# Performance work log

Hardware: AMD Instinct MI355X
Metric: run time of the kernel (lower is better)

The kernel has to match this reference:

```python
import math
import jax, jax.numpy as jnp
import numpy as np

B, S, E, H = 2, 2048, 1024, 16
DK = E // H

def setup_inputs() -> dict:
    key = jax.random.key(0)
    ks = jax.random.split(key, 12)
    sc = 1.0 / math.sqrt(E)
    return {
        "x": jax.random.normal(ks[0], (B, S, E), jnp.float32),
        "kv": jax.random.normal(ks[1], (B, S, E), jnp.float32),
        "mask": jax.random.randint(ks[2], (B, S), 0, 2, jnp.int32),
        "attn_bias": jax.random.normal(ks[3], (B, S, S), jnp.float32),
        "WQ_w": jax.random.normal(ks[4], (E, E), jnp.float32) * sc,
        "WQ_b": jnp.zeros((E,), jnp.float32),
        "WK_w": jax.random.normal(ks[5], (E, E), jnp.float32) * sc,
        "WK_b": jnp.zeros((E,), jnp.float32),
        "WV_w": jax.random.normal(ks[6], (E, E), jnp.float32) * sc,
        "WV_b": jnp.zeros((E,), jnp.float32),
        "WO_w": jax.random.normal(ks[7], (E, E), jnp.float32) * sc,
        "WO_b": jnp.zeros((E,), jnp.float32),
    }

def reference(x, kv, mask, attn_bias, WQ_w, WQ_b, WK_w, WK_b, WV_w, WV_b, WO_w, WO_b):
    b, sq, _ = x.shape
    sk = kv.shape[1]
    # projections, split heads: [B,S,E] -> [B,H,S,DK]
    Q = (x @ WQ_w.T + WQ_b).reshape(b, sq, H, DK).transpose(0, 2, 1, 3)
    K = (kv @ WK_w.T + WK_b).reshape(b, sk, H, DK).transpose(0, 2, 1, 3)
    V = (kv @ WV_w.T + WV_b).reshape(b, sk, H, DK).transpose(0, 2, 1, 3)
    # scores [B,H,Sq,Sk]
    T = jnp.einsum('bhqd,bhkd->bhqk', Q, K) / math.sqrt(DK)
    T = T + attn_bias[:, None, :, :]  # 3D bias broadcast over heads
    m2 = jnp.einsum('bi,bj->bij', mask.astype(T.dtype), mask.astype(T.dtype))
    T = jnp.where(m2[:, None, :, :] == 0, jnp.asarray(-1e9, T.dtype), T)
    A = jax.nn.softmax(T, axis=-1)
    out = jnp.einsum('bhqk,bhkd->bhqd', A, V)  # [B,H,Sq,DK]
    out = out.transpose(0, 2, 1, 3).reshape(b, sq, E)
    return out @ WO_w.T + WO_b
```

## Files before the change

### kernel.cpp

```cpp
#include <hip/hip_runtime.h>

#define DEV static __device__ __forceinline__

typedef __attribute__((ext_vector_type(8))) __bf16 bf16x8;
typedef __attribute__((ext_vector_type(4))) float f32x4;

constexpr int CB = 2;
constexpr int CS = 2048;
constexpr int CE = 1024;
constexpr int CH = 16;
constexpr int CD = 64;
constexpr float LOG2E = 1.44269504f;

DEV unsigned short f2bf(float x) {
  unsigned int u = __float_as_uint(x);
  u += 0x7fffu + ((u >> 16) & 1u);
  return (unsigned short)(u >> 16);
}

DEV f32x4 mfma32(bf16x8 a, bf16x8 b, f32x4 c) {
  return __builtin_amdgcn_mfma_f32_16x16x32_bf16(a, b, c, 0, 0, 0);
}

DEV unsigned int cvtpk(float lo, float hi) {
  unsigned int r;
  asm("v_cvt_pk_bf16_f32 %0, %1, %2" : "=v"(r) : "v"(lo), "v"(hi));
  return r;
}

DEV float exp2r(float x) {
#if __has_builtin(__builtin_amdgcn_exp2f)
  return __builtin_amdgcn_exp2f(x);
#else
  float r; asm("v_exp_f32 %0, %1" : "=v"(r) : "v"(x)); return r;
#endif
}

DEV f32x4 unpk(unsigned int a, unsigned int b) {
  f32x4 r;
  r[0] = __uint_as_float(a << 16);
  r[1] = __uint_as_float(a & 0xffff0000u);
  r[2] = __uint_as_float(b << 16);
  r[3] = __uint_as_float(b & 0xffff0000u);
  return r;
}

DEV void stage16(const void* g, void* l) {
  __builtin_amdgcn_global_load_lds(
      (const __attribute__((address_space(1))) unsigned int*)g,
      (__attribute__((address_space(3))) unsigned int*)l, 16, 0, 0);
}

DEV void wcvt_body(long i, const float* __restrict__ w0, const float* __restrict__ w1,
                   const float* __restrict__ w2, const float* __restrict__ w3,
                   unsigned short* __restrict__ out) {
  const long WE = (long)CE * CE;
  const int wi = (int)(i >> 20);
  const float* src = wi == 0 ? w0 : wi == 1 ? w1 : wi == 2 ? w2 : w3;
  const long off = i & (WE - 1);
  float4 a = *reinterpret_cast<const float4*>(src + off);
  float4 b = *reinterpret_cast<const float4*>(src + off + 4);
  uint4 v;
  v.x = cvtpk(a.x, a.y); v.y = cvtpk(a.z, a.w);
  v.z = cvtpk(b.x, b.y); v.w = cvtpk(b.z, b.w);
  *reinterpret_cast<uint4*>(out + i) = v;
}

DEV void mbias_body(long idx, const float* __restrict__ bias, const int* __restrict__ mask,
                    unsigned short* __restrict__ mb16) {
  const int b = (int)(idx >> 22);
  const int q = (int)((idx >> 11) & (CS - 1));
  const int k0 = (int)(idx & (CS - 1));
  const bool mq = mask[b * CS + q] != 0;
  const int4 mk0 = *reinterpret_cast<const int4*>(mask + b * CS + k0);
  const int4 mk1 = *reinterpret_cast<const int4*>(mask + b * CS + k0 + 4);
  const float4 b0 = *reinterpret_cast<const float4*>(bias + idx);
  const float4 b1 = *reinterpret_cast<const float4*>(bias + idx + 4);
  const float NEG = -1e9f * LOG2E;
  float v[8];
  if (mq) {
    v[0] = (mk0.x != 0) ? b0.x * LOG2E : NEG;
    v[1] = (mk0.y != 0) ? b0.y * LOG2E : NEG;
    v[2] = (mk0.z != 0) ? b0.z * LOG2E : NEG;
    v[3] = (mk0.w != 0) ? b0.w * LOG2E : NEG;
    v[4] = (mk1.x != 0) ? b1.x * LOG2E : NEG;
    v[5] = (mk1.y != 0) ? b1.y * LOG2E : NEG;
    v[6] = (mk1.z != 0) ? b1.z * LOG2E : NEG;
    v[7] = (mk1.w != 0) ? b1.w * LOG2E : NEG;
  } else {
#pragma unroll
    for (int j = 0; j < 8; j++) v[j] = 0.f;
  }
  uint4 o;
  o.x = cvtpk(v[0], v[1]); o.y = cvtpk(v[2], v[3]);
  o.z = cvtpk(v[4], v[5]); o.w = cvtpk(v[6], v[7]);
  *reinterpret_cast<uint4*>(mb16 + idx) = o;
}

__global__ __launch_bounds__(256) void prep_all(const float* __restrict__ w0,
                                                const float* __restrict__ w1,
                                                const float* __restrict__ w2,
                                                const float* __restrict__ w3,
                                                unsigned short* __restrict__ wout,
                                                const float* __restrict__ bias,
                                                const int* __restrict__ mask,
                                                unsigned short* __restrict__ mb16) {
  const long WCB = (4L * CE * CE) / 2048;
  if (blockIdx.x < WCB) {
    wcvt_body(((long)blockIdx.x * 256 + threadIdx.x) * 8, w0, w1, w2, w3, wout);
  } else {
    mbias_body(((long)(blockIdx.x - WCB) * 256 + threadIdx.x) * 8, bias, mask, mb16);
  }
}

__global__ __launch_bounds__(512) void gemm_qkv(const float* __restrict__ xf,
                                                const float* __restrict__ kvf,
                                                const unsigned short* __restrict__ Wall,
                                                const float* __restrict__ bq,
                                                const float* __restrict__ bk,
                                                const float* __restrict__ bv,
                                                unsigned short* __restrict__ Qb) {
  __shared__ __align__(16) unsigned char ldsA[32768];
  __shared__ __align__(16) unsigned char ldsB[32768];
  const long NE = (long)CB * CS * CE;
  const long WE = (long)CE * CE;
  const int which = blockIdx.y >> 2;
  const int n0 = (blockIdx.y & 3) * 256;
  const int m0 = blockIdx.x * 256;
  const float* Ax = which == 0 ? xf : kvf;
  const unsigned char* Bb = (const unsigned char*)(Wall + (long)which * WE);
  const float* bias = which == 0 ? bq : which == 1 ? bk : bv;

  const int tid = threadIdx.x;
  const int lane = tid & 63, w = tid >> 6;
  const int wr = w >> 2, wc = w & 3;
  const int g = lane >> 4, rr = lane & 15;

  const int srow = tid >> 2;
  const int ecol = ((tid & 3) * 8) ^ (((tid >> 5) & 1) * 16);
  const float* afp0 = Ax + (long)(m0 + srow) * CE + ecol;
  const float* afp1 = Ax + (long)(m0 + 128 + srow) * CE + ecol;
  const float* afb0 = afp0;
  const float* afb1 = afp1;
  const int scsw = ((tid & 3) * 16) ^ (((tid >> 5) & 1) << 5);
  const unsigned char* bpR0 = Bb + ((long)(n0 + srow) * CE) * 2 + scsw;
  const unsigned char* bpR1 = Bb + ((long)(n0 + 128 + srow) * CE) * 2 + scsw;

  const int cswz = (g * 16) ^ (((rr >> 3) & 1) << 5);
  const unsigned char* rbA = ldsA + wr * 8192 + rr * 64 + cswz;
  const unsigned char* rbB = ldsB + wc * 4096 + rr * 64 + cswz;

  f32x4 acc[8][4] = {};
  float4 afr0, afr1, afr2, afr3;

  auto loadA = [&](bool junk) {
    const float* p0 = junk ? afb0 : afp0;
    const float* p1 = junk ? afb1 : afp1;
    afr0 = *reinterpret_cast<const float4*>(p0);
    afr1 = *reinterpret_cast<const float4*>(p0 + 4);
    afr2 = *reinterpret_cast<const float4*>(p1);
    afr3 = *reinterpret_cast<const float4*>(p1 + 4);
    if (!junk) { afp0 += 32; afp1 += 32; }
  };
  auto writeA = [&](int buf) {
    uint4 w0v, w1v;
    w0v.x = cvtpk(afr0.x, afr0.y); w0v.y = cvtpk(afr0.z, afr0.w);
    w0v.z = cvtpk(afr1.x, afr1.y); w0v.w = cvtpk(afr1.z, afr1.w);
    w1v.x = cvtpk(afr2.x, afr2.y); w1v.y = cvtpk(afr2.z, afr2.w);
    w1v.z = cvtpk(afr3.x, afr3.y); w1v.w = cvtpk(afr3.z, afr3.w);
    *reinterpret_cast<uint4*>(ldsA + buf * 16384 + tid * 16) = w0v;
    *reinterpret_cast<uint4*>(ldsA + buf * 16384 + 8192 + tid * 16) = w1v;
  };
  auto stB = [&](int buf) {
    stage16(bpR0, ldsB + buf * 16384 + w * 1024);
    stage16(bpR1, ldsB + buf * 16384 + 8192 + w * 1024);
    bpR0 += 64; bpR1 += 64;
  };

  loadA(false);
  stB(0);
  asm volatile("s_waitcnt vmcnt(2)" ::: "memory");
  writeA(0);
  loadA(false);
  stB(1);
  asm volatile("s_waitcnt vmcnt(6)" ::: "memory");
  asm volatile("s_waitcnt lgkmcnt(0)" ::: "memory");
  __builtin_amdgcn_s_barrier();

  auto group = [&](int buf, bool junk) {
    bf16x8 ar[4], br[4];
#pragma unroll
    for (int ii = 0; ii < 4; ii++)
      ar[ii] = *reinterpret_cast<const bf16x8*>(rbA + buf * 16384 + ii * 1024);
#pragma unroll
    for (int j = 0; j < 4; j++)
      br[j] = *reinterpret_cast<const bf16x8*>(rbB + buf * 16384 + j * 1024);
    asm volatile("s_waitcnt vmcnt(2)" ::: "memory");
    writeA(buf ^ 1);
    loadA(junk);
    asm volatile("s_waitcnt lgkmcnt(0)" ::: "memory");
    __builtin_amdgcn_sched_barrier(0);
    __builtin_amdgcn_s_setprio(1);
#pragma unroll
    for (int ii = 0; ii < 4; ii++)
#pragma unroll
      for (int j = 0; j < 4; j++)
        acc[ii][j] = mfma32(ar[ii], br[j], acc[ii][j]);
    __builtin_amdgcn_s_setprio(0);
    __builtin_amdgcn_s_barrier();
#pragma unroll
    for (int ii = 0; ii < 4; ii++)
      ar[ii] = *reinterpret_cast<const bf16x8*>(rbA + buf * 16384 + 4096 + ii * 1024);
    stB(buf);
    asm volatile("s_waitcnt lgkmcnt(0)" ::: "memory");
    __builtin_amdgcn_sched_barrier(0);
    __builtin_amdgcn_s_setprio(1);
#pragma unroll
    for (int ii = 0; ii < 4; ii++)
#pragma unroll
      for (int j = 0; j < 4; j++)
        acc[4 + ii][j] = mfma32(ar[ii], br[j], acc[4 + ii][j]);
    __builtin_amdgcn_s_setprio(0);
    asm volatile("s_waitcnt vmcnt(6)" ::: "memory");
    __builtin_amdgcn_s_barrier();
  };

#pragma unroll 1
  for (int it = 0; it < 16; ++it) {
    group(0, it == 15);
    group(1, it == 15);
  }
  asm volatile("s_waitcnt vmcnt(0)" ::: "memory");

  const float scale = which == 0 ? 0.125f * LOG2E : 1.0f;
#pragma unroll
  for (int i = 0; i < 8; i++) {
#pragma unroll
    for (int j = 0; j < 4; j++) {
      const int colg = n0 + wc * 64 + j * 16 + rr;
      const float bvv = bias[colg];
      if (which == 2) {
        const int rowbase = m0 + wr * 128 + i * 16 + g * 4;
        const int bb = rowbase >> 11, s = rowbase & 2047;
        const int hh = colg >> 6, d = colg & 63;
        uint2 val;
        val.x = (unsigned int)f2bf(acc[i][j][0] + bvv) | ((unsigned int)f2bf(acc[i][j][1] + bvv) << 16);
        val.y = (unsigned int)f2bf(acc[i][j][2] + bvv) | ((unsigned int)f2bf(acc[i][j][3] + bvv) << 16);
        *reinterpret_cast<uint2*>(Qb + 2 * NE + ((long)((bb * CH + hh) * CD + d)) * CS + s) = val;
      } else {
        unsigned short* outp = Qb + (long)which * NE;
#pragma unroll
        for (int r = 0; r < 4; r++) {
          const int row = m0 + wr * 128 + i * 16 + g * 4 + r;
          outp[(long)row * CE + colg] = f2bf((acc[i][j][r] + bvv) * scale);
        }
      }
    }
  }
}

__global__ __launch_bounds__(256) void gemm_wo(const unsigned short* __restrict__ A,
                                               const unsigned short* __restrict__ W,
                                               const float* __restrict__ bias,
                                               float* __restrict__ out) {
  __shared__ __align__(16) unsigned short As[128 * 64];
  __shared__ __align__(16) unsigned short Bs[64 * 64];
  const int tid = threadIdx.x;
  const int lane = tid & 63, wave = tid >> 6;
  const int wm = (wave >> 1) * 64, wn = (wave & 1) * 32;
  const int g = lane >> 4, rr = lane & 15;
  const int m0 = blockIdx.x * 128, n0 = blockIdx.y * 64;
  const int K = CE;
  f32x4 acc[4][2] = {};

  for (int k0 = 0; k0 < K; k0 += 64) {
#pragma unroll
    for (int t = 0; t < 4; t++) {
      const int u = t * 256 + tid;
      const int row = u >> 3, ce = (u & 7) * 8;
      stage16(A + (long)(m0 + row) * K + k0 + ce, (char*)As + (t * 256 + (tid & 192)) * 16);
    }
#pragma unroll
    for (int t = 0; t < 2; t++) {
      const int u = t * 256 + tid;
      const int row = u >> 3, ce = (u & 7) * 8;
      stage16(W + (long)(n0 + row) * K + k0 + ce, (char*)Bs + (t * 256 + (tid & 192)) * 16);
    }
    __syncthreads();
#pragma unroll
    for (int kk = 0; kk < 2; kk++) {
      bf16x8 af[4], bfr[2];
#pragma unroll
      for (int i = 0; i < 4; i++)
        af[i] = *reinterpret_cast<const bf16x8*>(&As[(wm + i * 16 + rr) * 64 + kk * 32 + g * 8]);
#pragma unroll
      for (int j = 0; j < 2; j++)
        bfr[j] = *reinterpret_cast<const bf16x8*>(&Bs[(wn + j * 16 + rr) * 64 + kk * 32 + g * 8]);
#pragma unroll
      for (int i = 0; i < 4; i++)
#pragma unroll
        for (int j = 0; j < 2; j++)
          acc[i][j] = mfma32(af[i], bfr[j], acc[i][j]);
    }
    __syncthreads();
  }

#pragma unroll
  for (int i = 0; i < 4; i++)
#pragma unroll
    for (int j = 0; j < 2; j++) {
      const int colg = n0 + wn + j * 16 + rr;
      const float bvv = bias[colg];
#pragma unroll
      for (int r = 0; r < 4; r++) {
        const int row = m0 + wm + i * 16 + g * 4 + r;
        out[(long)row * CE + colg] = acc[i][j][r] + bvv;
      }
    }
}

__global__ __launch_bounds__(256, 2) void attn_kernel(const unsigned short* __restrict__ Qb,
                                                      const unsigned short* __restrict__ Kb,
                                                      const unsigned short* __restrict__ Vtw,
                                                      const unsigned short* __restrict__ mb16,
                                                      const int* __restrict__ mask,
                                                      unsigned short* __restrict__ AO) {
  __shared__ __align__(16) unsigned char lds[65536];
  const int h = blockIdx.x, qt = blockIdx.y, b = blockIdx.z;
  const int tid = threadIdx.x;
  const int lane = tid & 63, w = tid >> 6;
  const int g = lane >> 4, c = lane & 15;
  const int qbase = qt * 128 + w * 32;

  bf16x8 qf[2][2];
#pragma unroll
  for (int qb = 0; qb < 2; qb++) {
    const unsigned short* Qrow = Qb + ((long)b * CS + qbase + qb * 16 + c) * CE + h * CD;
    qf[qb][0] = *reinterpret_cast<const bf16x8*>(Qrow + g * 8);
    qf[qb][1] = *reinterpret_cast<const bf16x8*>(Qrow + 32 + g * 8);
    if (mask[b * CS + qbase + qb * 16 + c] == 0) {
      qf[qb][0] = bf16x8{}; qf[qb][1] = bf16x8{};
    }
  }

  const unsigned char *kg[4], *vg[4];
  {
    const unsigned char* Ksrc = (const unsigned char*)(Kb + (long)b * CS * CE + h * CD);
    const unsigned char* Vsrc = (const unsigned char*)(Vtw + (long)(b * CH + h) * CD * CS);
    const int rr8 = lane >> 3;
    const int csw = ((lane & 7) << 4) ^ (rr8 << 4);
#pragma unroll
    for (int t = 0; t < 4; t++) {
      const int krow = t * 32 + w * 8 + rr8;
      const int key = (krow & 96) + ((krow >> 2) & 3) * 8 + ((krow >> 4) & 1) * 4 + (krow & 3);
      kg[t] = Ksrc + (long)key * (CE * 2) + csw;
      const int vrow = (t & 1) * 32 + w * 8 + rr8;
      vg[t] = Vsrc + (long)vrow * (CS * 2) + (t >> 1) * 128 + csw;
    }
  }
  const int sw = (c & 7) << 4;
  const unsigned char* rb0 = lds + c * 128 + ((g * 16) ^ sw);
  const unsigned char* rb1 = lds + c * 128 + ((64 + g * 16) ^ sw);

  const unsigned short* mbp0 = mb16 + ((long)b * CS + qbase + c) * CS + g * 8;
  const unsigned short* mbp1 = mb16 + ((long)b * CS + qbase + 16 + c) * CS + g * 8;

  f32x4 o[2][4] = {};
  f32x4 lsum4[2] = {};
  uint4 mbr[2][4];

  auto stage = [&](int bo) {
    unsigned char* kbuf = lds + bo;
    unsigned char* vbuf = lds + bo + 16384;
#pragma unroll
    for (int t = 0; t < 4; t++) {
      stage16(kg[t], kbuf + t * 4096 + w * 1024);
      stage16(vg[t], vbuf + (t >> 1) * 8192 + (t & 1) * 4096 + w * 1024);
      kg[t] += 128 * CE * 2;
      vg[t] += 128 * 2;
    }
  };
  auto load_mb = [&](bool adv) {
#pragma unroll
    for (int kb = 0; kb < 4; kb++) {
      mbr[0][kb] = *reinterpret_cast<const uint4*>(mbp0 + kb * 32);
      mbr[1][kb] = *reinterpret_cast<const uint4*>(mbp1 + kb * 32);
    }
    if (adv) { mbp0 += 128; mbp1 += 128; }
  };

  auto compute = [&](int bo, bool adv) {
    f32x4 sf[2][8];
    __builtin_amdgcn_s_setprio(1);
#pragma unroll
    for (int cb = 0; cb < 8; cb++) {
      const bf16x8 kf0 = *reinterpret_cast<const bf16x8*>(rb0 + bo + cb * 2048);
      const bf16x8 kf1 = *reinterpret_cast<const bf16x8*>(rb1 + bo + cb * 2048);
#pragma unroll
      for (int qb = 0; qb < 2; qb++) {
        const uint4 m = mbr[qb][cb >> 1];
        const f32x4 ci = (cb & 1) ? unpk(m.z, m.w) : unpk(m.x, m.y);
        f32x4 t = mfma32(kf0, qf[qb][0], ci);
        sf[qb][cb] = mfma32(kf1, qf[qb][1], t);
      }
    }
    __builtin_amdgcn_s_setprio(0);
    load_mb(adv);
    uint4 pw[2][4];
#pragma unroll
    for (int qb = 0; qb < 2; qb++)
#pragma unroll
      for (int kb = 0; kb < 4; kb++)
#pragma unroll
        for (int half = 0; half < 2; half++) {
          const int cb = 2 * kb + half;
          f32x4 pv;
          pv[0] = exp2r(sf[qb][cb][0]);
          pv[1] = exp2r(sf[qb][cb][1]);
          pv[2] = exp2r(sf[qb][cb][2]);
          pv[3] = exp2r(sf[qb][cb][3]);
          lsum4[qb] = lsum4[qb] + pv;
          if (half == 0) { pw[qb][kb].x = cvtpk(pv[0], pv[1]); pw[qb][kb].y = cvtpk(pv[2], pv[3]); }
          else           { pw[qb][kb].z = cvtpk(pv[0], pv[1]); pw[qb][kb].w = cvtpk(pv[2], pv[3]); }
        }
    __builtin_amdgcn_s_setprio(1);
#pragma unroll
    for (int nb = 0; nb < 4; nb++) {
#pragma unroll
      for (int kb = 0; kb < 4; kb++) {
        const unsigned char* rbx = (kb & 1) ? rb1 : rb0;
        const bf16x8 vf = *reinterpret_cast<const bf16x8*>(
            rbx + bo + 16384 + (kb >> 1) * 8192 + nb * 2048);
#pragma unroll
        for (int qb = 0; qb < 2; qb++)
          o[qb][nb] = mfma32(vf, __builtin_bit_cast(bf16x8, pw[qb][kb]), o[qb][nb]);
      }
    }
    __builtin_amdgcn_s_setprio(0);
  };

  stage(0);
  load_mb(true);
  stage(32768);

#pragma unroll 1
  for (int it = 0; it < 8; ++it) {
    asm volatile("s_waitcnt vmcnt(16)" ::: "memory");
    __builtin_amdgcn_s_barrier();
    __builtin_amdgcn_sched_barrier(0);
    compute(0, it < 7);
    __builtin_amdgcn_sched_barrier(0);
    __builtin_amdgcn_s_barrier();
    stage(0);
    asm volatile("s_waitcnt vmcnt(16)" ::: "memory");
    __builtin_amdgcn_s_barrier();
    __builtin_amdgcn_sched_barrier(0);
    compute(32768, it < 7);
    __builtin_amdgcn_sched_barrier(0);
    __builtin_amdgcn_s_barrier();
    stage(32768);
  }

#pragma unroll
  for (int qb = 0; qb < 2; qb++) {
    float lsum = (lsum4[qb][0] + lsum4[qb][1]) + (lsum4[qb][2] + lsum4[qb][3]);
    lsum += __shfl_xor(lsum, 16, 64);
    lsum += __shfl_xor(lsum, 32, 64);
    const float linv = 1.0f / lsum;
    unsigned short* Orow = AO + ((long)b * CS + qbase + qb * 16 + c) * CE + h * CD;
#pragma unroll
    for (int nb = 0; nb < 4; nb++) {
      uint2 val;
      val.x = (unsigned int)f2bf(o[qb][nb][0] * linv) | ((unsigned int)f2bf(o[qb][nb][1] * linv) << 16);
      val.y = (unsigned int)f2bf(o[qb][nb][2] * linv) | ((unsigned int)f2bf(o[qb][nb][3] * linv) << 16);
      *reinterpret_cast<uint2*>(Orow + nb * 16 + g * 4) = val;
    }
  }
  asm volatile("s_waitcnt vmcnt(0)" ::: "memory");
}

extern "C" void kernel_launch(void* const* d_in, const int* in_sizes, int n_in,
                              void* d_out, int out_size, void* d_ws, size_t ws_size,
                              hipStream_t stream) {
  (void)in_sizes; (void)n_in; (void)out_size; (void)ws_size;
  const float* x    = (const float*)d_in[0];
  const float* kv   = (const float*)d_in[1];
  const int*   mask = (const int*)d_in[2];
  const float* ab   = (const float*)d_in[3];
  const float* WQw  = (const float*)d_in[4];
  const float* WQb  = (const float*)d_in[5];
  const float* WKw  = (const float*)d_in[6];
  const float* WKb  = (const float*)d_in[7];
  const float* WVw  = (const float*)d_in[8];
  const float* WVb  = (const float*)d_in[9];
  const float* WOw  = (const float*)d_in[10];
  const float* WOb  = (const float*)d_in[11];
  float* out = (float*)d_out;

  const long NE = (long)CB * CS * CE;
  const long WE = (long)CE * CE;
  unsigned short* ws  = (unsigned short*)d_ws;
  unsigned short* wqb = ws;
  unsigned short* wob = wqb + 3 * WE;
  unsigned short* Qb  = wob + WE;
  unsigned short* AO  = Qb + 3 * NE;
  unsigned short* mb16 = AO + NE;

  const long WCE = 4 * WE;
  const long MBE = (long)CB * CS * CS;

  prep_all<<<(int)((WCE + MBE) / 2048), 256, 0, stream>>>(WQw, WKw, WVw, WOw, wqb,
                                                          ab, mask, mb16);

  gemm_qkv<<<dim3(16, 12), 512, 0, stream>>>(x, kv, wqb, WQb, WKb, WVb, Qb);

  attn_kernel<<<dim3(CH, CS / 128, CB), 256, 0, stream>>>(
      Qb, Qb + NE, Qb + 2 * NE, mb16, mask, AO);

  gemm_wo<<<dim3(32, 16), 256, 0, stream>>>(AO, wob, WOb, out);
}
```

Baseline: 132.0 us.

## Fuse mask and bias into attention kernel, dropping the precomputed bf16 bias buffer

Removes the prep pass that built a pre-scaled, pre-masked bf16 bias matrix. The attention kernel now reads the fp32 attention bias and the key mask directly and applies the scale, mask and query-mask select before exp2, instead of seeding the MFMA accumulator with the bias. This saves one full write and read of a B×S×S buffer plus its prep launch. In exchange, every head block now reads fp32 bias, twice the bytes of bf16, and does extra ALU work per score. The prefetch and wait schedule for the bias loads is also simplified, so load latency may be exposed inside compute.

```diff
diff --git a/kernel.cpp b/kernel.cpp
--- a/kernel.cpp
+++ b/kernel.cpp
@@ -36,25 +36,19 @@
 #endif
 }
 
-DEV f32x4 unpk(unsigned int a, unsigned int b) {
-  f32x4 r;
-  r[0] = __uint_as_float(a << 16);
-  r[1] = __uint_as_float(a & 0xffff0000u);
-  r[2] = __uint_as_float(b << 16);
-  r[3] = __uint_as_float(b & 0xffff0000u);
-  return r;
-}
-
 DEV void stage16(const void* g, void* l) {
   __builtin_amdgcn_global_load_lds(
       (const __attribute__((address_space(1))) unsigned int*)g,
       (__attribute__((address_space(3))) unsigned int*)l, 16, 0, 0);
 }
 
-DEV void wcvt_body(long i, const float* __restrict__ w0, const float* __restrict__ w1,
-                   const float* __restrict__ w2, const float* __restrict__ w3,
-                   unsigned short* __restrict__ out) {
+__global__ __launch_bounds__(256) void wcvt_all(const float* __restrict__ w0,
+                                                const float* __restrict__ w1,
+                                                const float* __restrict__ w2,
+                                                const float* __restrict__ w3,
+                                                unsigned short* __restrict__ out) {
   const long WE = (long)CE * CE;
+  const long i = ((long)blockIdx.x * 256 + threadIdx.x) * 8;
   const int wi = (int)(i >> 20);
   const float* src = wi == 0 ? w0 : wi == 1 ? w1 : wi == 2 ? w2 : w3;
   const long off = i & (WE - 1);
@@ -64,53 +58,6 @@
   v.x = cvtpk(a.x, a.y); v.y = cvtpk(a.z, a.w);
   v.z = cvtpk(b.x, b.y); v.w = cvtpk(b.z, b.w);
   *reinterpret_cast<uint4*>(out + i) = v;
-}
-
-DEV void mbias_body(long idx, const float* __restrict__ bias, const int* __restrict__ mask,
-                    unsigned short* __restrict__ mb16) {
-  const int b = (int)(idx >> 22);
-  const int q = (int)((idx >> 11) & (CS - 1));
-  const int k0 = (int)(idx & (CS - 1));
-  const bool mq = mask[b * CS + q] != 0;
-  const int4 mk0 = *reinterpret_cast<const int4*>(mask + b * CS + k0);
-  const int4 mk1 = *reinterpret_cast<const int4*>(mask + b * CS + k0 + 4);
-  const float4 b0 = *reinterpret_cast<const float4*>(bias + idx);
-  const float4 b1 = *reinterpret_cast<const float4*>(bias + idx + 4);
-  const float NEG = -1e9f * LOG2E;
-  float v[8];
-  if (mq) {
-    v[0] = (mk0.x != 0) ? b0.x * LOG2E : NEG;
-    v[1] = (mk0.y != 0) ? b0.y * LOG2E : NEG;
-    v[2] = (mk0.z != 0) ? b0.z * LOG2E : NEG;
-    v[3] = (mk0.w != 0) ? b0.w * LOG2E : NEG;
-    v[4] = (mk1.x != 0) ? b1.x * LOG2E : NEG;
-    v[5] = (mk1.y != 0) ? b1.y * LOG2E : NEG;
-    v[6] = (mk1.z != 0) ? b1.z * LOG2E : NEG;
-    v[7] = (mk1.w != 0) ? b1.w * LOG2E : NEG;
-  } else {
-#pragma unroll
-    for (int j = 0; j < 8; j++) v[j] = 0.f;
-  }
-  uint4 o;
-  o.x = cvtpk(v[0], v[1]); o.y = cvtpk(v[2], v[3]);
-  o.z = cvtpk(v[4], v[5]); o.w = cvtpk(v[6], v[7]);
-  *reinterpret_cast<uint4*>(mb16 + idx) = o;
-}
-
-__global__ __launch_bounds__(256) void prep_all(const float* __restrict__ w0,
-                                                const float* __restrict__ w1,
-                                                const float* __restrict__ w2,
-                                                const float* __restrict__ w3,
-                                                unsigned short* __restrict__ wout,
-                                                const float* __restrict__ bias,
-                                                const int* __restrict__ mask,
-                                                unsigned short* __restrict__ mb16) {
-  const long WCB = (4L * CE * CE) / 2048;
-  if (blockIdx.x < WCB) {
-    wcvt_body(((long)blockIdx.x * 256 + threadIdx.x) * 8, w0, w1, w2, w3, wout);
-  } else {
-    mbias_body(((long)(blockIdx.x - WCB) * 256 + threadIdx.x) * 8, bias, mask, mb16);
-  }
 }
 
 __global__ __launch_bounds__(512) void gemm_qkv(const float* __restrict__ xf,
@@ -322,7 +269,7 @@
 __global__ __launch_bounds__(256, 2) void attn_kernel(const unsigned short* __restrict__ Qb,
                                                       const unsigned short* __restrict__ Kb,
                                                       const unsigned short* __restrict__ Vtw,
-                                                      const unsigned short* __restrict__ mb16,
+                                                      const float* __restrict__ bias,
                                                       const int* __restrict__ mask,
                                                       unsigned short* __restrict__ AO) {
   __shared__ __align__(16) unsigned char lds[65536];
@@ -333,14 +280,14 @@
   const int qbase = qt * 128 + w * 32;
 
   bf16x8 qf[2][2];
+  bool mq[2];
 #pragma unroll
   for (int qb = 0; qb < 2; qb++) {
     const unsigned short* Qrow = Qb + ((long)b * CS + qbase + qb * 16 + c) * CE + h * CD;
     qf[qb][0] = *reinterpret_cast<const bf16x8*>(Qrow + g * 8);
     qf[qb][1] = *reinterpret_cast<const bf16x8*>(Qrow + 32 + g * 8);
-    if (mask[b * CS + qbase + qb * 16 + c] == 0) {
-      qf[qb][0] = bf16x8{}; qf[qb][1] = bf16x8{};
-    }
+    mq[qb] = mask[b * CS + qbase + qb * 16 + c] != 0;
+    if (!mq[qb]) { qf[qb][0] = bf16x8{}; qf[qb][1] = bf16x8{}; }
   }
 
   const unsigned char *kg[4], *vg[4];
@@ -362,12 +309,12 @@
   const unsigned char* rb0 = lds + c * 128 + ((g * 16) ^ sw);
   const unsigned char* rb1 = lds + c * 128 + ((64 + g * 16) ^ sw);
 
-  const unsigned short* mbp0 = mb16 + ((long)b * CS + qbase + c) * CS + g * 8;
-  const unsigned short* mbp1 = mb16 + ((long)b * CS + qbase + 16 + c) * CS + g * 8;
+  const float* bp0 = bias + ((long)b * CS + qbase + c) * CS + g * 8;
+  const float* bp1 = bias + ((long)b * CS + qbase + 16 + c) * CS + g * 8;
+  const int* mp = mask + b * CS + g * 8;
 
   f32x4 o[2][4] = {};
   f32x4 lsum4[2] = {};
-  uint4 mbr[2][4];
 
   auto stage = [&](int bo) {
     unsigned char* kbuf = lds + bo;
@@ -380,16 +327,20 @@
       vg[t] += 128 * 2;
     }
   };
-  auto load_mb = [&](bool adv) {
+
+  auto compute = [&](int bo) {
+    float4 bf[2][4][2];
+    int4 mi[4][2];
 #pragma unroll
     for (int kb = 0; kb < 4; kb++) {
-      mbr[0][kb] = *reinterpret_cast<const uint4*>(mbp0 + kb * 32);
-      mbr[1][kb] = *reinterpret_cast<const uint4*>(mbp1 + kb * 32);
-    }
-    if (adv) { mbp0 += 128; mbp1 += 128; }
-  };
-
-  auto compute = [&](int bo, bool adv) {
+      bf[0][kb][0] = *reinterpret_cast<const float4*>(bp0 + kb * 32);
+      bf[0][kb][1] = *reinterpret_cast<const float4*>(bp0 + kb * 32 + 4);
+      bf[1][kb][0] = *reinterpret_cast<const float4*>(bp1 + kb * 32);
+      bf[1][kb][1] = *reinterpret_cast<const float4*>(bp1 + kb * 32 + 4);
+      mi[kb][0] = *reinterpret_cast<const int4*>(mp + kb * 32);
+      mi[kb][1] = *reinterpret_cast<const int4*>(mp + kb * 32 + 4);
+    }
+    bp0 += 128; bp1 += 128; mp += 128;
     f32x4 sf[2][8];
     __builtin_amdgcn_s_setprio(1);
 #pragma unroll
@@ -398,14 +349,13 @@
       const bf16x8 kf1 = *reinterpret_cast<const bf16x8*>(rb1 + bo + cb * 2048);
 #pragma unroll
       for (int qb = 0; qb < 2; qb++) {
-        const uint4 m = mbr[qb][cb >> 1];
-        const f32x4 ci = (cb & 1) ? unpk(m.z, m.w) : unpk(m.x, m.y);
-        f32x4 t = mfma32(kf0, qf[qb][0], ci);
+        f32x4 t = mfma32(kf0, qf[qb][0], f32x4{});
         sf[qb][cb] = mfma32(kf1, qf[qb][1], t);
       }
     }
     __builtin_amdgcn_s_setprio(0);
-    load_mb(adv);
+    __builtin_amdgcn_sched_barrier(0);
+    const float NEGC = -1e9f * LOG2E;
     uint4 pw[2][4];
 #pragma unroll
     for (int qb = 0; qb < 2; qb++)
@@ -414,11 +364,18 @@
 #pragma unroll
         for (int half = 0; half < 2; half++) {
           const int cb = 2 * kb + half;
+          const float4 bv = bf[qb][kb][half];
+          const int4 mk = mi[kb][half];
+          const float bvs[4] = {bv.x, bv.y, bv.z, bv.w};
+          const int mks[4] = {mk.x, mk.y, mk.z, mk.w};
           f32x4 pv;
-          pv[0] = exp2r(sf[qb][cb][0]);
-          pv[1] = exp2r(sf[qb][cb][1]);
-          pv[2] = exp2r(sf[qb][cb][2]);
-          pv[3] = exp2r(sf[qb][cb][3]);
+#pragma unroll
+          for (int r = 0; r < 4; r++) {
+            float t = fmaf(bvs[r], LOG2E, sf[qb][cb][r]);
+            t = (mks[r] != 0) ? t : NEGC;
+            t = mq[qb] ? t : sf[qb][cb][r];
+            pv[r] = exp2r(t);
+          }
           lsum4[qb] = lsum4[qb] + pv;
           if (half == 0) { pw[qb][kb].x = cvtpk(pv[0], pv[1]); pw[qb][kb].y = cvtpk(pv[2], pv[3]); }
           else           { pw[qb][kb].z = cvtpk(pv[0], pv[1]); pw[qb][kb].w = cvtpk(pv[2], pv[3]); }
@@ -440,23 +397,16 @@
   };
 
   stage(0);
-  load_mb(true);
   stage(32768);
+  asm volatile("s_waitcnt vmcnt(8)" ::: "memory");
+  __builtin_amdgcn_s_barrier();
 
 #pragma unroll 1
   for (int it = 0; it < 8; ++it) {
-    asm volatile("s_waitcnt vmcnt(16)" ::: "memory");
-    __builtin_amdgcn_s_barrier();
-    __builtin_amdgcn_sched_barrier(0);
-    compute(0, it < 7);
-    __builtin_amdgcn_sched_barrier(0);
+    compute(0);
     __builtin_amdgcn_s_barrier();
     stage(0);
-    asm volatile("s_waitcnt vmcnt(16)" ::: "memory");
-    __builtin_amdgcn_s_barrier();
-    __builtin_amdgcn_sched_barrier(0);
-    compute(32768, it < 7);
-    __builtin_amdgcn_sched_barrier(0);
+    compute(32768);
     __builtin_amdgcn_s_barrier();
     stage(32768);
   }
@@ -504,18 +454,13 @@
   unsigned short* wob = wqb + 3 * WE;
   unsigned short* Qb  = wob + WE;
   unsigned short* AO  = Qb + 3 * NE;
-  unsigned short* mb16 = AO + NE;
-
-  const long WCE = 4 * WE;
-  const long MBE = (long)CB * CS * CS;
-
-  prep_all<<<(int)((WCE + MBE) / 2048), 256, 0, stream>>>(WQw, WKw, WVw, WOw, wqb,
-                                                          ab, mask, mb16);
+
+  wcvt_all<<<(int)((4 * WE) / 2048), 256, 0, stream>>>(WQw, WKw, WVw, WOw, wqb);
 
   gemm_qkv<<<dim3(16, 12), 512, 0, stream>>>(x, kv, wqb, WQb, WKb, WVb, Qb);
 
   attn_kernel<<<dim3(CH, CS / 128, CB), 256, 0, stream>>>(
-      Qb, Qb + NE, Qb + 2 * NE, mb16, mask, AO);
+      Qb, Qb + NE, Qb + 2 * NE, ab, mask, AO);
 
   gemm_wo<<<dim3(32, 16), 256, 0, stream>>>(AO, wob, WOb, out);
 }
```

Measured after the change: 191.9 us. +45.4%, slower.

## Overlap mask-bias preparation with QKV GEMM in one launch

Applied to the files above, without the earlier changes.

Splits the combined prep kernel so that weight conversion runs alone, and moves the mask/bias bf16 preparation into extra blocks of the QKV GEMM launch (a 1D grid of 192 GEMM blocks plus 2048 bias blocks). The goal is to overlap the bandwidth-bound bias pass with the compute-bound GEMM, since the GEMM's 192 blocks do not fill the GPU. The trade-off is that the bias blocks now carry the GEMM kernel's 64KB LDS allocation and 512-thread shape, which may limit how many can be resident at once and could delay the GEMM blocks.

```diff
diff --git a/kernel.cpp b/kernel.cpp
--- a/kernel.cpp
+++ b/kernel.cpp
@@ -51,10 +51,13 @@
       (__attribute__((address_space(3))) unsigned int*)l, 16, 0, 0);
 }
 
-DEV void wcvt_body(long i, const float* __restrict__ w0, const float* __restrict__ w1,
-                   const float* __restrict__ w2, const float* __restrict__ w3,
-                   unsigned short* __restrict__ out) {
+__global__ __launch_bounds__(256) void wcvt_all(const float* __restrict__ w0,
+                                                const float* __restrict__ w1,
+                                                const float* __restrict__ w2,
+                                                const float* __restrict__ w3,
+                                                unsigned short* __restrict__ out) {
   const long WE = (long)CE * CE;
+  const long i = ((long)blockIdx.x * 256 + threadIdx.x) * 8;
   const int wi = (int)(i >> 20);
   const float* src = wi == 0 ? w0 : wi == 1 ? w1 : wi == 2 ? w2 : w3;
   const long off = i & (WE - 1);
@@ -66,8 +69,8 @@
   *reinterpret_cast<uint4*>(out + i) = v;
 }
 
-DEV void mbias_body(long idx, const float* __restrict__ bias, const int* __restrict__ mask,
-                    unsigned short* __restrict__ mb16) {
+DEV void mbias_body512(long idx, const float* __restrict__ bias, const int* __restrict__ mask,
+                       unsigned short* __restrict__ mb16) {
   const int b = (int)(idx >> 22);
   const int q = (int)((idx >> 11) & (CS - 1));
   const int k0 = (int)(idx & (CS - 1));
@@ -97,41 +100,34 @@
   *reinterpret_cast<uint4*>(mb16 + idx) = o;
 }
 
-__global__ __launch_bounds__(256) void prep_all(const float* __restrict__ w0,
-                                                const float* __restrict__ w1,
-                                                const float* __restrict__ w2,
-                                                const float* __restrict__ w3,
-                                                unsigned short* __restrict__ wout,
-                                                const float* __restrict__ bias,
-                                                const int* __restrict__ mask,
-                                                unsigned short* __restrict__ mb16) {
-  const long WCB = (4L * CE * CE) / 2048;
-  if (blockIdx.x < WCB) {
-    wcvt_body(((long)blockIdx.x * 256 + threadIdx.x) * 8, w0, w1, w2, w3, wout);
-  } else {
-    mbias_body(((long)(blockIdx.x - WCB) * 256 + threadIdx.x) * 8, bias, mask, mb16);
-  }
-}
-
 __global__ __launch_bounds__(512) void gemm_qkv(const float* __restrict__ xf,
                                                 const float* __restrict__ kvf,
                                                 const unsigned short* __restrict__ Wall,
                                                 const float* __restrict__ bq,
                                                 const float* __restrict__ bk,
                                                 const float* __restrict__ bv,
-                                                unsigned short* __restrict__ Qb) {
+                                                unsigned short* __restrict__ Qb,
+                                                const float* __restrict__ bias,
+                                                const int* __restrict__ mask,
+                                                unsigned short* __restrict__ mb16) {
   __shared__ __align__(16) unsigned char ldsA[32768];
   __shared__ __align__(16) unsigned char ldsB[32768];
+  const int bx = blockIdx.x;
+  const int tid = threadIdx.x;
+  if (bx >= 192) {
+    mbias_body512(((long)(bx - 192) * 512 + tid) * 8, bias, mask, mb16);
+    return;
+  }
   const long NE = (long)CB * CS * CE;
   const long WE = (long)CE * CE;
-  const int which = blockIdx.y >> 2;
-  const int n0 = (blockIdx.y & 3) * 256;
-  const int m0 = blockIdx.x * 256;
+  const int mx = bx & 15, ny = bx >> 4;
+  const int which = ny >> 2;
+  const int n0 = (ny & 3) * 256;
+  const int m0 = mx * 256;
   const float* Ax = which == 0 ? xf : kvf;
   const unsigned char* Bb = (const unsigned char*)(Wall + (long)which * WE);
-  const float* bias = which == 0 ? bq : which == 1 ? bk : bv;
-
-  const int tid = threadIdx.x;
+  const float* bq_ = which == 0 ? bq : which == 1 ? bk : bv;
+
   const int lane = tid & 63, w = tid >> 6;
   const int wr = w >> 2, wc = w & 3;
   const int g = lane >> 4, rr = lane & 15;
@@ -238,7 +234,7 @@
 #pragma unroll
     for (int j = 0; j < 4; j++) {
       const int colg = n0 + wc * 64 + j * 16 + rr;
-      const float bvv = bias[colg];
+      const float bvv = bq_[colg];
       if (which == 2) {
         const int rowbase = m0 + wr * 128 + i * 16 + g * 4;
         const int bb = rowbase >> 11, s = rowbase & 2047;
@@ -506,13 +502,10 @@
   unsigned short* AO  = Qb + 3 * NE;
   unsigned short* mb16 = AO + NE;
 
-  const long WCE = 4 * WE;
-  const long MBE = (long)CB * CS * CS;
-
-  prep_all<<<(int)((WCE + MBE) / 2048), 256, 0, stream>>>(WQw, WKw, WVw, WOw, wqb,
-                                                          ab, mask, mb16);
-
-  gemm_qkv<<<dim3(16, 12), 512, 0, stream>>>(x, kv, wqb, WQb, WKb, WVb, Qb);
+  wcvt_all<<<(int)((4 * WE) / 2048), 256, 0, stream>>>(WQw, WKw, WVw, WOw, wqb);
+
+  gemm_qkv<<<dim3(192 + 2048), 512, 0, stream>>>(x, kv, wqb, WQb, WKb, WVb, Qb,
+                                                 ab, mask, mb16);
 
   attn_kernel<<<dim3(CH, CS / 128, CB), 256, 0, stream>>>(
       Qb, Qb + NE, Qb + 2 * NE, mb16, mask, AO);
```

Result: faster. 128.7 us (-2.5%).
